# Kernel tuning notes

Measured on AMD Instinct MI355X. Metric: run time of the kernel, lower is better.

## Reference

```python
import jax, jax.numpy as jnp
import numpy as np

B, D_IN, D_EMB = 8192, 256, 128
N_EX, N_DUR = 16384, 64
N_TRAIN = 100000
THRESH = 1.0


def setup_inputs() -> dict:
    key = jax.random.key(0)
    ks = jax.random.split(key, 6)
    x = jax.random.normal(ks[0], (B, D_IN), jnp.float32)
    # small scales so pairwise distances straddle the threshold (realistic kernel regime)
    W = jax.random.normal(ks[1], (D_IN, D_EMB), jnp.float32) * 0.003
    b = jnp.zeros((D_EMB,), jnp.float32)
    E = jax.random.normal(ks[2], (N_EX, D_EMB), jnp.float32) * 0.05
    log_ev = jax.random.normal(ks[3], (N_EX, N_DUR), jnp.float32)
    log_cen = jax.random.normal(ks[4], (N_EX, N_DUR), jnp.float32)
    logit_h = jax.random.normal(ks[5], (N_DUR,), jnp.float32) - 3.0
    return {
        "input": x, "W": W, "b": b, "exemplar_embeddings": E,
        "log_exemplar_event_counts": log_ev,
        "log_exemplar_censor_counts": log_cen,
        "logit_baseline_hazard": logit_h,
    }


def _kernel_weights(x, W, b, E):
    # encoder (no_grad in original): single linear layer
    phi = x @ W + b  # [B, D_EMB]
    # cdist via Gram expansion; clamp tiny negatives from roundoff
    d2 = (jnp.sum(phi * phi, axis=1, keepdims=True)
          + jnp.sum(E * E, axis=1)[None, :]
          - 2.0 * (phi @ E.T))
    d2 = jnp.maximum(d2, 0.0)          # [B, N_EX] squared distances
    d = jnp.sqrt(d2)
    # threshold mask + exp kernel (matches exp(-distance**2))
    return jnp.where(d <= THRESH, jnp.exp(-d2), 0.0)


def reference(input, W, b, exemplar_embeddings,
              log_exemplar_event_counts, log_exemplar_censor_counts,
              logit_baseline_hazard):
    kw = jax.lax.stop_gradient(
        _kernel_weights(input, W, b, exemplar_embeddings))  # [B, N_EX]

    baseline_hazard = jax.nn.sigmoid(logit_baseline_hazard)  # [N_DUR]
    baseline_KM = jnp.exp(jnp.cumsum(jnp.log(1.0 - baseline_hazard + 1e-7)))

    ev = jnp.exp(log_exemplar_event_counts)    # [N_EX, N_DUR]
    cen = jnp.exp(log_exemplar_censor_counts)  # [N_EX, N_DUR]
    # reverse cumulative sum along durations = flip/cumsum/flip
    at_risk = jnp.flip(jnp.cumsum(jnp.flip(ev + cen, axis=1), axis=1), axis=1)
    pos = at_risk > 0
    hazards = jnp.where(pos, ev / jnp.where(pos, at_risk, 1.0), 0.0)
    exemplar_KM = jnp.exp(jnp.cumsum(jnp.log(1.0 - hazards + 1e-7), axis=1))

    gamma_n = jnp.exp(-(THRESH ** 2)) / N_TRAIN
    numer = kw @ exemplar_KM + gamma_n * baseline_KM[None, :]  # [B, N_DUR]
    denom = (jnp.sum(kw, axis=1) + gamma_n + 1e-12)[:, None]
    return jnp.clip(numer / denom, 1e-12, 1.0 - 1e-12)
```

## Files before the change

kernel.cpp:

```cpp
#include <hip/hip_runtime.h>

using short8  = __attribute__((ext_vector_type(8))) short;
using floatx4 = __attribute__((ext_vector_type(4))) float;

#define NB   8192
#define DIN  256
#define DE   128
#define NEX  16384
#define ND   64
#define ESPLIT 16
#define EPB  (NEX/ESPLIT)
#define TE   64
#define NTIL (EPB/TE)
#define GAMMA_N 3.6787944117144233e-06f

__device__ __forceinline__ unsigned short f2bf(float f) {
  unsigned int u = __float_as_uint(f);
  u += 0x7fffu + ((u >> 16) & 1u);
  return (unsigned short)(u >> 16);
}
__device__ __forceinline__ float bf2f(unsigned short h) {
  return __uint_as_float(((unsigned int)h) << 16);
}
__device__ __forceinline__ unsigned int pk_bf16(float a, float b) {
  unsigned int r;
  asm("v_cvt_pk_bf16_f32 %0, %1, %2" : "=v"(r) : "v"(a), "v"(b));
  return r;
}

__device__ __forceinline__ void gload_lds16(const void* g, void* l) {
  __builtin_amdgcn_global_load_lds(
      (const __attribute__((address_space(1))) void*)g,
      (__attribute__((address_space(3))) void*)l, 16, 0, 0);
}

__device__ __forceinline__ floatx4 mfma_bf16(short8 a, short8 b, floatx4 c) {
  return __builtin_amdgcn_mfma_f32_16x16x32_bf16(a, b, c, 0, 0, 0);
}

__global__ __launch_bounds__(256) void k_encoder(
    const float* __restrict__ x, const float* __restrict__ W,
    const float* __restrict__ bias, unsigned short* __restrict__ phi_bf,
    float* __restrict__ pn)
{
  __shared__ float xs[32 * DIN];
  const int rb  = blockIdx.x * 32;
  const int tid = threadIdx.x;
  for (int i = tid; i < 32 * DIN / 4; i += 256)
    reinterpret_cast<float4*>(xs)[i] =
        reinterpret_cast<const float4*>(x + (size_t)rb * DIN)[i];
  __syncthreads();
  const int jt = tid & 31;
  const int rt = tid >> 5;
  const float4 bj = *reinterpret_cast<const float4*>(&bias[jt * 4]);
  float4 a0 = bj, a1 = bj, a2 = bj, a3 = bj;
  const float* xr = xs + rt * 4 * DIN;
  #pragma unroll 4
  for (int k = 0; k < DIN; ++k) {
    const float4 wv = *reinterpret_cast<const float4*>(&W[k * DE + jt * 4]);
    const float x0 = xr[k], x1 = xr[DIN + k], x2 = xr[2 * DIN + k], x3 = xr[3 * DIN + k];
    a0.x = fmaf(x0, wv.x, a0.x); a0.y = fmaf(x0, wv.y, a0.y);
    a0.z = fmaf(x0, wv.z, a0.z); a0.w = fmaf(x0, wv.w, a0.w);
    a1.x = fmaf(x1, wv.x, a1.x); a1.y = fmaf(x1, wv.y, a1.y);
    a1.z = fmaf(x1, wv.z, a1.z); a1.w = fmaf(x1, wv.w, a1.w);
    a2.x = fmaf(x2, wv.x, a2.x); a2.y = fmaf(x2, wv.y, a2.y);
    a2.z = fmaf(x2, wv.z, a2.z); a2.w = fmaf(x2, wv.w, a2.w);
    a3.x = fmaf(x3, wv.x, a3.x); a3.y = fmaf(x3, wv.y, a3.y);
    a3.z = fmaf(x3, wv.z, a3.z); a3.w = fmaf(x3, wv.w, a3.w);
  }
  float4 av[4] = {a0, a1, a2, a3};
  #pragma unroll
  for (int rr = 0; rr < 4; ++rr) {
    const int row = rb + rt * 4 + rr;
    const unsigned int p0 = pk_bf16(av[rr].x, av[rr].y);
    const unsigned int p1 = pk_bf16(av[rr].z, av[rr].w);
    *reinterpret_cast<uint2*>(phi_bf + (size_t)row * DE + jt * 4) =
        make_uint2(p0, p1);
    const float h0 = bf2f(p0 & 0xffff), h1 = bf2f(p0 >> 16);
    const float h2 = bf2f(p1 & 0xffff), h3 = bf2f(p1 >> 16);
    float s = h0 * h0 + h1 * h1 + h2 * h2 + h3 * h3;
    s += __shfl_xor(s, 1, 64);
    s += __shfl_xor(s, 2, 64);
    s += __shfl_xor(s, 4, 64);
    s += __shfl_xor(s, 8, 64);
    s += __shfl_xor(s, 16, 64);
    if (jt == 0) pn[row] = s;
  }
}

__global__ __launch_bounds__(256) void k_prep_e(
    const float* __restrict__ E, unsigned short* __restrict__ E_bf,
    float* __restrict__ en)
{
  const int tid = threadIdx.x;
  const int w = tid >> 6, l = tid & 63;
  const int row = blockIdx.x * 32 + w * 8 + (l >> 3);
  const int c0  = (l & 7) * 16;
  const float4* src = reinterpret_cast<const float4*>(E + (size_t)row * DE + c0);
  float4 v0 = src[0], v1 = src[1], v2 = src[2], v3 = src[3];
  unsigned int p[8];
  p[0] = pk_bf16(v0.x, v0.y); p[1] = pk_bf16(v0.z, v0.w);
  p[2] = pk_bf16(v1.x, v1.y); p[3] = pk_bf16(v1.z, v1.w);
  p[4] = pk_bf16(v2.x, v2.y); p[5] = pk_bf16(v2.z, v2.w);
  p[6] = pk_bf16(v3.x, v3.y); p[7] = pk_bf16(v3.z, v3.w);
  uint4* dst = reinterpret_cast<uint4*>(E_bf + (size_t)row * DE + c0);
  dst[0] = make_uint4(p[0], p[1], p[2], p[3]);
  dst[1] = make_uint4(p[4], p[5], p[6], p[7]);
  float s = 0.f;
  #pragma unroll
  for (int i = 0; i < 8; ++i) {
    const float lo = bf2f(p[i] & 0xffff), hi = bf2f(p[i] >> 16);
    s = fmaf(lo, lo, s); s = fmaf(hi, hi, s);
  }
  s += __shfl_xor(s, 1, 64);
  s += __shfl_xor(s, 2, 64);
  s += __shfl_xor(s, 4, 64);
  if ((l & 7) == 0) en[row] = s;
}

__global__ __launch_bounds__(256) void k_prep_km(
    const float* __restrict__ lev, const float* __restrict__ lcen,
    const float* __restrict__ lh, unsigned short* __restrict__ KM_t,
    float* __restrict__ baseKM)
{
  __shared__ unsigned short sm[64][65];
  const int tid = threadIdx.x;
  const int t   = tid & 63;
  const int wv  = tid >> 6;
  for (int ee = 0; ee < 16; ++ee) {
    const int el = wv * 16 + ee;
    const int e  = blockIdx.x * 64 + el;
    const float ev = __expf(lev[e * ND + t]);
    const float cn = __expf(lcen[e * ND + t]);
    float s = ev + cn;
    #pragma unroll
    for (int off = 1; off < 64; off <<= 1) {
      const float o = __shfl(s, (t + off) & 63, 64);
      s += (t + off < 64) ? o : 0.0f;
    }
    const float haz = (s > 0.0f) ? (ev / s) : 0.0f;
    float lc = __logf(1.0f - haz + 1e-7f);
    #pragma unroll
    for (int off = 1; off < 64; off <<= 1) {
      const float o = __shfl(lc, (t - off) & 63, 64);
      lc += (t >= off) ? o : 0.0f;
    }
    sm[el][t] = f2bf(__expf(lc));
  }
  __syncthreads();
  const int t_out = tid >> 2, prt = tid & 3;
  unsigned short tmp[16];
  #pragma unroll
  for (int i = 0; i < 16; ++i) tmp[i] = sm[prt * 16 + i][t_out];
  *reinterpret_cast<short8*>(KM_t + (size_t)t_out * NEX + blockIdx.x * 64 + prt * 16) =
      *reinterpret_cast<short8*>(&tmp[0]);
  *reinterpret_cast<short8*>(KM_t + (size_t)t_out * NEX + blockIdx.x * 64 + prt * 16 + 8) =
      *reinterpret_cast<short8*>(&tmp[8]);
  if (blockIdx.x == 0 && tid < 64) {
    const float h = 1.0f / (1.0f + __expf(-lh[t]));
    float l2 = __logf(1.0f - h + 1e-7f);
    #pragma unroll
    for (int off = 1; off < 64; off <<= 1) {
      const float o = __shfl(l2, (t - off) & 63, 64);
      l2 += (t >= off) ? o : 0.0f;
    }
    baseKM[t] = __expf(l2);
  }
}

__global__ __launch_bounds__(256, 4) void k_fused(
    const unsigned short* __restrict__ phi_bf, const float* __restrict__ pn,
    const unsigned short* __restrict__ E_bf, const float* __restrict__ en,
    const unsigned short* __restrict__ KM_t,
    float* __restrict__ numer_p, float* __restrict__ denom_p)
{
  __shared__ __align__(16) unsigned char E_lds[16384];
  __shared__ __align__(16) unsigned char KM_lds[8192];
  __shared__ __align__(16) unsigned char kw_lds[8192];

  const int tid = threadIdx.x;
  const int w   = tid >> 6;
  const int l   = tid & 63;
  const int lr  = l & 15;
  const int g   = l >> 4;
  const int rowbase = blockIdx.y * 128 + w * 32;
  const int ebase0  = blockIdx.x * EPB;
  const int swz  = (lr & 7) << 4;
  const int swz2 = ((lr >> 1) & 3) << 4;

  short8 phiB[2][4];
  float  pnf[2];
  #pragma unroll
  for (int n = 0; n < 2; ++n) {
    const int r = rowbase + n * 16 + lr;
    #pragma unroll
    for (int kq = 0; kq < 4; ++kq)
      phiB[n][kq] = *reinterpret_cast<const short8*>(phi_bf + r * DE + kq * 32 + g * 8);
    pnf[n] = pn[r];
  }

  floatx4 c2[4][2];
  #pragma unroll
  for (int m2 = 0; m2 < 4; ++m2)
    #pragma unroll
    for (int n = 0; n < 2; ++n) c2[m2][n] = (floatx4){0.f, 0.f, 0.f, 0.f};
  float dn[2] = {0.f, 0.f};

  for (int it = 0; it < NTIL; ++it) {
    const int ebase = ebase0 + it * TE;
    __syncthreads();
    #pragma unroll
    for (int i = 0; i < 4; ++i) {
      const int c    = w * 4 + i;
      const int row  = c * 4 + (l >> 4);
      const int colB = (l & 15) * 16;
      gload_lds16((const char*)E_bf + (size_t)(ebase + row) * 256 +
                      (colB ^ ((row & 7) << 4)),
                  &E_lds[c * 1024]);
    }
    #pragma unroll
    for (int i = 0; i < 2; ++i) {
      const int c    = w * 2 + i;
      const int trow = c * 8 + (l >> 3);
      const int colB = (l & 7) * 16;
      gload_lds16((const char*)KM_t + (size_t)trow * (NEX * 2) + ebase * 2 +
                      (colB ^ ((trow & 7) << 4)),
                  &KM_lds[c * 1024]);
    }
    __syncthreads();

    #pragma unroll
    for (int h = 0; h < 2; ++h) {
      #pragma unroll
      for (int mm = 0; mm < 2; ++mm) {
        const int m = 2 * h + mm;
        short8 ea[4];
        #pragma unroll
        for (int kq = 0; kq < 4; ++kq)
          ea[kq] = *reinterpret_cast<const short8*>(
              &E_lds[(m * 16 + lr) * 256 + ((kq * 64 + g * 16) ^ swz)]);
        floatx4 c1[2];
        c1[0] = (floatx4){0.f, 0.f, 0.f, 0.f};
        c1[1] = (floatx4){0.f, 0.f, 0.f, 0.f};
        #pragma unroll
        for (int kq = 0; kq < 4; ++kq) {
          c1[0] = mfma_bf16(ea[kq], phiB[0][kq], c1[0]);
          c1[1] = mfma_bf16(ea[kq], phiB[1][kq], c1[1]);
        }
        const floatx4 en4 = *reinterpret_cast<const floatx4*>(&en[ebase + m * 16 + g * 4]);
        #pragma unroll
        for (int n = 0; n < 2; ++n) {
          float kwv[4];
          #pragma unroll
          for (int rg = 0; rg < 4; ++rg) {
            const float d2 = en4[rg] + pnf[n] - 2.0f * c1[n][rg];
            kwv[rg] = (d2 <= 1.0f) ? __expf(-d2) : 0.0f;
            dn[n] += kwv[rg];
          }
          const unsigned int pk0 = pk_bf16(kwv[0], kwv[1]);
          const unsigned int pk1 = pk_bf16(kwv[2], kwv[3]);
          const unsigned long long pk = (unsigned long long)pk0 |
                                        ((unsigned long long)pk1 << 32);
          *reinterpret_cast<unsigned long long*>(
              &kw_lds[w * 2048 + (n * 16 + lr) * 64 + ((mm * 32 + g * 8) ^ swz2)]) = pk;
        }
      }
      short8 kwB[2];
      #pragma unroll
      for (int n = 0; n < 2; ++n)
        kwB[n] = *reinterpret_cast<const short8*>(
            &kw_lds[w * 2048 + (n * 16 + lr) * 64 + ((g * 16) ^ swz2)]);
      #pragma unroll
      for (int m2 = 0; m2 < 4; ++m2) {
        const short8 kma = *reinterpret_cast<const short8*>(
            &KM_lds[(m2 * 16 + lr) * 128 + ((h * 64 + g * 16) ^ swz)]);
        c2[m2][0] = mfma_bf16(kma, kwB[0], c2[m2][0]);
        c2[m2][1] = mfma_bf16(kma, kwB[1], c2[m2][1]);
      }
    }
  }

  #pragma unroll
  for (int n = 0; n < 2; ++n) {
    float v = dn[n];
    v += __shfl_xor(v, 16, 64);
    v += __shfl_xor(v, 32, 64);
    if (l < 16) denom_p[(size_t)blockIdx.x * NB + rowbase + n * 16 + lr] = v;
  }
  float* np = numer_p + ((size_t)blockIdx.x * NB + rowbase) * ND;
  #pragma unroll
  for (int n = 0; n < 2; ++n)
    #pragma unroll
    for (int m2 = 0; m2 < 4; ++m2)
      *reinterpret_cast<floatx4*>(&np[(n * 16 + lr) * ND + m2 * 16 + g * 4]) =
          c2[m2][n];
}

__global__ __launch_bounds__(256) void k_finalize(
    const float* __restrict__ numer_p, const float* __restrict__ denom_p,
    const float* __restrict__ baseKM, float* __restrict__ out)
{
  const int idx = blockIdx.x * 256 + threadIdx.x;
  const int b = idx >> 6;
  const int t = idx & 63;
  float num = 0.f, den = 0.f;
  #pragma unroll
  for (int s = 0; s < ESPLIT; ++s) {
    num += numer_p[(size_t)s * NB * ND + idx];
    den += denom_p[(size_t)s * NB + b];
  }
  num += GAMMA_N * baseKM[t];
  den += GAMMA_N + 1e-12f;
  float r = num / den;
  r = fminf(fmaxf(r, 1e-12f), 1.0f - 1e-12f);
  out[idx] = r;
}

extern "C" void kernel_launch(void* const* d_in, const int* in_sizes, int n_in,
                              void* d_out, int out_size, void* d_ws, size_t ws_size,
                              hipStream_t stream)
{
  const float* x    = (const float*)d_in[0];
  const float* W    = (const float*)d_in[1];
  const float* bias = (const float*)d_in[2];
  const float* E    = (const float*)d_in[3];
  const float* lev  = (const float*)d_in[4];
  const float* lcen = (const float*)d_in[5];
  const float* lh   = (const float*)d_in[6];
  float* out = (float*)d_out;

  char* ws = (char*)d_ws;
  size_t off = 0;
  auto alloc = [&](size_t bytes) -> void* {
    void* p = ws + off;
    off += (bytes + 255) & ~(size_t)255;
    return p;
  };
  unsigned short* phi_bf  = (unsigned short*)alloc((size_t)NB * DE * 2);
  unsigned short* E_bf    = (unsigned short*)alloc((size_t)NEX * DE * 2);
  unsigned short* KM_t    = (unsigned short*)alloc((size_t)ND * NEX * 2);
  float* pn       = (float*)alloc((size_t)NB * 4);
  float* en       = (float*)alloc((size_t)NEX * 4);
  float* baseKM   = (float*)alloc((size_t)ND * 4);
  float* numer_p  = (float*)alloc((size_t)ESPLIT * NB * ND * 4);
  float* denom_p  = (float*)alloc((size_t)ESPLIT * NB * 4);

  k_encoder<<<NB / 32, 256, 0, stream>>>(x, W, bias, phi_bf, pn);
  k_prep_e<<<NEX / 32, 256, 0, stream>>>(E, E_bf, en);
  k_prep_km<<<NEX / 64, 256, 0, stream>>>(lev, lcen, lh, KM_t, baseKM);
  k_fused<<<dim3(ESPLIT, NB / 128), 256, 0, stream>>>(phi_bf, pn, E_bf, en, KM_t,
                                                      numer_p, denom_p);
  k_finalize<<<(NB * ND) / 256, 256, 0, stream>>>(numer_p, denom_p, baseKM, out);
}
```

Measured before the change: 197.3 us.

## Merge encoder, exemplar prep and KM prep into one block-partitioned kernel

Replaces three separate prep launches with a single kernel whose block index selects among the encoder, exemplar bf16 conversion and Kaplan-Meier prep branches. The encoder now computes one row per thread-group (8 rows per block, 1024 blocks) instead of four, and KM prep handles 32 exemplars per block, so blocks are smaller, more numerous and use less LDS. This removes two launch gaps and lets the independent prep stages run concurrently, at the cost of less register reuse of W loads in the encoder.

```diff
diff --git a/kernel.cpp b/kernel.cpp
--- a/kernel.cpp
+++ b/kernel.cpp
@@ -38,42 +38,41 @@
   return __builtin_amdgcn_mfma_f32_16x16x32_bf16(a, b, c, 0, 0, 0);
 }
 
-__global__ __launch_bounds__(256) void k_encoder(
+__global__ __launch_bounds__(256) void k_prep(
     const float* __restrict__ x, const float* __restrict__ W,
     const float* __restrict__ bias, unsigned short* __restrict__ phi_bf,
-    float* __restrict__ pn)
+    float* __restrict__ pn,
+    const float* __restrict__ E, unsigned short* __restrict__ E_bf,
+    float* __restrict__ en,
+    const float* __restrict__ lev, const float* __restrict__ lcen,
+    const float* __restrict__ lh, unsigned short* __restrict__ KM_t,
+    float* __restrict__ baseKM)
 {
-  __shared__ float xs[32 * DIN];
-  const int rb  = blockIdx.x * 32;
+  __shared__ __align__(16) unsigned char smem[8192];
+  const int bid = blockIdx.x;
   const int tid = threadIdx.x;
-  for (int i = tid; i < 32 * DIN / 4; i += 256)
-    reinterpret_cast<float4*>(xs)[i] =
-        reinterpret_cast<const float4*>(x + (size_t)rb * DIN)[i];
-  __syncthreads();
-  const int jt = tid & 31;
-  const int rt = tid >> 5;
-  const float4 bj = *reinterpret_cast<const float4*>(&bias[jt * 4]);
-  float4 a0 = bj, a1 = bj, a2 = bj, a3 = bj;
-  const float* xr = xs + rt * 4 * DIN;
-  #pragma unroll 4
-  for (int k = 0; k < DIN; ++k) {
-    const float4 wv = *reinterpret_cast<const float4*>(&W[k * DE + jt * 4]);
-    const float x0 = xr[k], x1 = xr[DIN + k], x2 = xr[2 * DIN + k], x3 = xr[3 * DIN + k];
-    a0.x = fmaf(x0, wv.x, a0.x); a0.y = fmaf(x0, wv.y, a0.y);
-    a0.z = fmaf(x0, wv.z, a0.z); a0.w = fmaf(x0, wv.w, a0.w);
-    a1.x = fmaf(x1, wv.x, a1.x); a1.y = fmaf(x1, wv.y, a1.y);
-    a1.z = fmaf(x1, wv.z, a1.z); a1.w = fmaf(x1, wv.w, a1.w);
-    a2.x = fmaf(x2, wv.x, a2.x); a2.y = fmaf(x2, wv.y, a2.y);
-    a2.z = fmaf(x2, wv.z, a2.z); a2.w = fmaf(x2, wv.w, a2.w);
-    a3.x = fmaf(x3, wv.x, a3.x); a3.y = fmaf(x3, wv.y, a3.y);
-    a3.z = fmaf(x3, wv.z, a3.z); a3.w = fmaf(x3, wv.w, a3.w);
-  }
-  float4 av[4] = {a0, a1, a2, a3};
-  #pragma unroll
-  for (int rr = 0; rr < 4; ++rr) {
-    const int row = rb + rt * 4 + rr;
-    const unsigned int p0 = pk_bf16(av[rr].x, av[rr].y);
-    const unsigned int p1 = pk_bf16(av[rr].z, av[rr].w);
+
+  if (bid < 1024) {
+    const int rb = bid * 8;
+    float* xs = (float*)smem;
+    for (int i = tid; i < 8 * DIN / 4; i += 256)
+      reinterpret_cast<float4*>(xs)[i] =
+          reinterpret_cast<const float4*>(x + (size_t)rb * DIN)[i];
+    __syncthreads();
+    const int jt = tid & 31;
+    const int rt = tid >> 5;
+    float4 acc = *reinterpret_cast<const float4*>(&bias[jt * 4]);
+    const float* xr = xs + rt * DIN;
+    #pragma unroll 8
+    for (int k = 0; k < DIN; ++k) {
+      const float4 wv = *reinterpret_cast<const float4*>(&W[k * DE + jt * 4]);
+      const float xv = xr[k];
+      acc.x = fmaf(xv, wv.x, acc.x); acc.y = fmaf(xv, wv.y, acc.y);
+      acc.z = fmaf(xv, wv.z, acc.z); acc.w = fmaf(xv, wv.w, acc.w);
+    }
+    const int row = rb + rt;
+    const unsigned int p0 = pk_bf16(acc.x, acc.y);
+    const unsigned int p1 = pk_bf16(acc.z, acc.w);
     *reinterpret_cast<uint2*>(phi_bf + (size_t)row * DE + jt * 4) =
         make_uint2(p0, p1);
     const float h0 = bf2f(p0 & 0xffff), h1 = bf2f(p0 >> 16);
@@ -85,86 +84,75 @@
     s += __shfl_xor(s, 8, 64);
     s += __shfl_xor(s, 16, 64);
     if (jt == 0) pn[row] = s;
-  }
-}
-
-__global__ __launch_bounds__(256) void k_prep_e(
-    const float* __restrict__ E, unsigned short* __restrict__ E_bf,
-    float* __restrict__ en)
-{
-  const int tid = threadIdx.x;
-  const int w = tid >> 6, l = tid & 63;
-  const int row = blockIdx.x * 32 + w * 8 + (l >> 3);
-  const int c0  = (l & 7) * 16;
-  const float4* src = reinterpret_cast<const float4*>(E + (size_t)row * DE + c0);
-  float4 v0 = src[0], v1 = src[1], v2 = src[2], v3 = src[3];
-  unsigned int p[8];
-  p[0] = pk_bf16(v0.x, v0.y); p[1] = pk_bf16(v0.z, v0.w);
-  p[2] = pk_bf16(v1.x, v1.y); p[3] = pk_bf16(v1.z, v1.w);
-  p[4] = pk_bf16(v2.x, v2.y); p[5] = pk_bf16(v2.z, v2.w);
-  p[6] = pk_bf16(v3.x, v3.y); p[7] = pk_bf16(v3.z, v3.w);
-  uint4* dst = reinterpret_cast<uint4*>(E_bf + (size_t)row * DE + c0);
-  dst[0] = make_uint4(p[0], p[1], p[2], p[3]);
-  dst[1] = make_uint4(p[4], p[5], p[6], p[7]);
-  float s = 0.f;
-  #pragma unroll
-  for (int i = 0; i < 8; ++i) {
-    const float lo = bf2f(p[i] & 0xffff), hi = bf2f(p[i] >> 16);
-    s = fmaf(lo, lo, s); s = fmaf(hi, hi, s);
-  }
-  s += __shfl_xor(s, 1, 64);
-  s += __shfl_xor(s, 2, 64);
-  s += __shfl_xor(s, 4, 64);
-  if ((l & 7) == 0) en[row] = s;
-}
-
-__global__ __launch_bounds__(256) void k_prep_km(
-    const float* __restrict__ lev, const float* __restrict__ lcen,
-    const float* __restrict__ lh, unsigned short* __restrict__ KM_t,
-    float* __restrict__ baseKM)
-{
-  __shared__ unsigned short sm[64][65];
-  const int tid = threadIdx.x;
-  const int t   = tid & 63;
-  const int wv  = tid >> 6;
-  for (int ee = 0; ee < 16; ++ee) {
-    const int el = wv * 16 + ee;
-    const int e  = blockIdx.x * 64 + el;
-    const float ev = __expf(lev[e * ND + t]);
-    const float cn = __expf(lcen[e * ND + t]);
-    float s = ev + cn;
-    #pragma unroll
-    for (int off = 1; off < 64; off <<= 1) {
-      const float o = __shfl(s, (t + off) & 63, 64);
-      s += (t + off < 64) ? o : 0.0f;
-    }
-    const float haz = (s > 0.0f) ? (ev / s) : 0.0f;
-    float lc = __logf(1.0f - haz + 1e-7f);
-    #pragma unroll
-    for (int off = 1; off < 64; off <<= 1) {
-      const float o = __shfl(lc, (t - off) & 63, 64);
-      lc += (t >= off) ? o : 0.0f;
-    }
-    sm[el][t] = f2bf(__expf(lc));
-  }
-  __syncthreads();
-  const int t_out = tid >> 2, prt = tid & 3;
-  unsigned short tmp[16];
-  #pragma unroll
-  for (int i = 0; i < 16; ++i) tmp[i] = sm[prt * 16 + i][t_out];
-  *reinterpret_cast<short8*>(KM_t + (size_t)t_out * NEX + blockIdx.x * 64 + prt * 16) =
-      *reinterpret_cast<short8*>(&tmp[0]);
-  *reinterpret_cast<short8*>(KM_t + (size_t)t_out * NEX + blockIdx.x * 64 + prt * 16 + 8) =
-      *reinterpret_cast<short8*>(&tmp[8]);
-  if (blockIdx.x == 0 && tid < 64) {
-    const float h = 1.0f / (1.0f + __expf(-lh[t]));
-    float l2 = __logf(1.0f - h + 1e-7f);
-    #pragma unroll
-    for (int off = 1; off < 64; off <<= 1) {
-      const float o = __shfl(l2, (t - off) & 63, 64);
-      l2 += (t >= off) ? o : 0.0f;
-    }
-    baseKM[t] = __expf(l2);
+
+  } else if (bid < 1536) {
+    const int bb = bid - 1024;
+    const int l  = tid & 63;
+    const int row = bb * 32 + (tid >> 6) * 8 + (l >> 3);
+    const int c0  = (l & 7) * 16;
+    const float4* src = reinterpret_cast<const float4*>(E + (size_t)row * DE + c0);
+    float4 v0 = src[0], v1 = src[1], v2 = src[2], v3 = src[3];
+    unsigned int p[8];
+    p[0] = pk_bf16(v0.x, v0.y); p[1] = pk_bf16(v0.z, v0.w);
+    p[2] = pk_bf16(v1.x, v1.y); p[3] = pk_bf16(v1.z, v1.w);
+    p[4] = pk_bf16(v2.x, v2.y); p[5] = pk_bf16(v2.z, v2.w);
+    p[6] = pk_bf16(v3.x, v3.y); p[7] = pk_bf16(v3.z, v3.w);
+    uint4* dst = reinterpret_cast<uint4*>(E_bf + (size_t)row * DE + c0);
+    dst[0] = make_uint4(p[0], p[1], p[2], p[3]);
+    dst[1] = make_uint4(p[4], p[5], p[6], p[7]);
+    float s = 0.f;
+    #pragma unroll
+    for (int i = 0; i < 8; ++i) {
+      const float lo = bf2f(p[i] & 0xffff), hi = bf2f(p[i] >> 16);
+      s = fmaf(lo, lo, s); s = fmaf(hi, hi, s);
+    }
+    s += __shfl_xor(s, 1, 64);
+    s += __shfl_xor(s, 2, 64);
+    s += __shfl_xor(s, 4, 64);
+    if ((l & 7) == 0) en[row] = s;
+
+  } else {
+    const int bb = bid - 1536;
+    unsigned short (*sm)[65] = (unsigned short (*)[65])smem;
+    const int t  = tid & 63;
+    const int wv = tid >> 6;
+    for (int ee = 0; ee < 8; ++ee) {
+      const int el = wv * 8 + ee;
+      const int e  = bb * 32 + el;
+      const float ev = __expf(lev[e * ND + t]);
+      const float cn = __expf(lcen[e * ND + t]);
+      float s = ev + cn;
+      #pragma unroll
+      for (int off = 1; off < 64; off <<= 1) {
+        const float o = __shfl(s, (t + off) & 63, 64);
+        s += (t + off < 64) ? o : 0.0f;
+      }
+      const float haz = (s > 0.0f) ? (ev / s) : 0.0f;
+      float lc = __logf(1.0f - haz + 1e-7f);
+      #pragma unroll
+      for (int off = 1; off < 64; off <<= 1) {
+        const float o = __shfl(lc, (t - off) & 63, 64);
+        lc += (t >= off) ? o : 0.0f;
+      }
+      sm[el][t] = f2bf(__expf(lc));
+    }
+    __syncthreads();
+    const int t_out = tid >> 2, prt = tid & 3;
+    unsigned short tmp[8];
+    #pragma unroll
+    for (int i = 0; i < 8; ++i) tmp[i] = sm[prt * 8 + i][t_out];
+    *reinterpret_cast<short8*>(KM_t + (size_t)t_out * NEX + bb * 32 + prt * 8) =
+        *reinterpret_cast<short8*>(&tmp[0]);
+    if (bb == 0 && tid < 64) {
+      const float h = 1.0f / (1.0f + __expf(-lh[t]));
+      float l2 = __logf(1.0f - h + 1e-7f);
+      #pragma unroll
+      for (int off = 1; off < 64; off <<= 1) {
+        const float o = __shfl(l2, (t - off) & 63, 64);
+        l2 += (t >= off) ? o : 0.0f;
+      }
+      baseKM[t] = __expf(l2);
+    }
   }
 }
 
@@ -345,9 +333,9 @@
   float* numer_p  = (float*)alloc((size_t)ESPLIT * NB * ND * 4);
   float* denom_p  = (float*)alloc((size_t)ESPLIT * NB * 4);
 
-  k_encoder<<<NB / 32, 256, 0, stream>>>(x, W, bias, phi_bf, pn);
-  k_prep_e<<<NEX / 32, 256, 0, stream>>>(E, E_bf, en);
-  k_prep_km<<<NEX / 64, 256, 0, stream>>>(lev, lcen, lh, KM_t, baseKM);
+  k_prep<<<2048, 256, 0, stream>>>(x, W, bias, phi_bf, pn,
+                                   E, E_bf, en,
+                                   lev, lcen, lh, KM_t, baseKM);
   k_fused<<<dim3(ESPLIT, NB / 128), 256, 0, stream>>>(phi_bf, pn, E_bf, en, KM_t,
                                                       numer_p, denom_p);
   k_finalize<<<(NB * ND) / 256, 256, 0, stream>>>(numer_p, denom_p, baseKM, out);
```

Measured after the change: 189.8 us. -3.8%, faster.
